# Kernel tuning notes

Measured on AMD Instinct MI355X. Metric: run time of the kernel, lower is better.

## Reference

```python
import jax, jax.numpy as jnp
import numpy as np
import math

T, N, D, H = 1024, 8, 1024, 16
HD = D // H  # head_dim = 64


def setup_inputs() -> dict:
    key = jax.random.key(0)
    k1, k2, k3, k4 = jax.random.split(key, 4)
    scale = 1.0 / math.sqrt(D)  # roughly xavier-scale params
    return {
        "x": jax.random.normal(k1, (T, N, D), dtype=jnp.float32),
        "q_weight": jax.random.normal(k2, (D, H, HD), dtype=jnp.float32) * scale,
        "v_weight": jax.random.normal(k3, (D, H, HD), dtype=jnp.float32) * scale,
        "out_w": jax.random.normal(k4, (D, D), dtype=jnp.float32) * scale,
        "out_b": jnp.zeros((D,), dtype=jnp.float32),
    }


def reference(x, q_weight, v_weight, out_w, out_b):
    inv_sqrt_hd = 1.0 / math.sqrt(HD)
    # q = k : (T, N, H, HD)
    q = jnp.einsum('tbm,mhd->tbhd', x, q_weight)
    q_sq = jnp.einsum('tbhd,tbhd->tbh', q, q)  # squared norms
    # squared L2 distance logits: (T, S, N, H)
    squared_dist = q_sq[:, None] + q_sq[None, :] - 2.0 * jnp.einsum('tbhd,sbhd->tsbh', q, q)
    attn_logits = -squared_dist * inv_sqrt_hd
    attn_weights = jax.nn.softmax(attn_logits, axis=1)  # softmax over source dim S
    # A = W_q W_q^T per head: (H, D, D)
    A = jnp.einsum('mhd,nhd->hmn', q_weight, q_weight) * inv_sqrt_hd
    XA = jnp.einsum('tbm,hmn->tbhn', x, A)           # (T, N, H, D)
    PXA = jnp.einsum('tsbh,sbhm->tbhm', attn_weights, XA)  # (T, N, H, D)
    PXAV = jnp.einsum('tbhm,mhd->tbhd', PXA, v_weight).reshape(T, N, D)
    return PXAV @ out_w.T + out_b
```

## Files before the change

### kernel.cpp

```cpp
#include <hip/hip_runtime.h>
#include <hip/hip_bf16.h>

#define T_ 1024
#define N_ 8
#define D_ 1024
#define H_ 16
#define HD_ 64

typedef __attribute__((ext_vector_type(8))) short bf16x8;
typedef __attribute__((ext_vector_type(2))) float f32x2;
typedef __attribute__((ext_vector_type(4))) float f32x4;
typedef __attribute__((ext_vector_type(16))) float f32x16;
typedef __attribute__((ext_vector_type(4))) int i32x4;
typedef __attribute__((ext_vector_type(2))) int i32x2;
typedef unsigned short u16;
typedef unsigned int u32;

__device__ __forceinline__ float bf2f(u16 u){
  union { float f; unsigned int i; } v; v.i = ((unsigned int)u) << 16; return v.f;
}
__device__ __forceinline__ u16 f2bf(float f){
  union { float f; unsigned int i; } v; v.f = f;
  unsigned int r = v.i + 0x7FFFu + ((v.i >> 16) & 1u);
  return (u16)(r >> 16);
}
__device__ __forceinline__ u16 f2bf_fast(float f){
  __hip_bfloat16 h = __float2bfloat16(f);
  return *reinterpret_cast<u16*>(&h);
}
__device__ __forceinline__ float exp2_raw(float x){
  float r;
  asm("v_exp_f32 %0, %1" : "=v"(r) : "v"(x));
  return r;
}
__device__ __forceinline__ void gl_lds16(const u16* g, u16* l){
  __builtin_amdgcn_global_load_lds(
      (const __attribute__((address_space(1))) unsigned int*)g,
      (__attribute__((address_space(3))) unsigned int*)(unsigned int)(unsigned long long)l,
      16, 0, 0);
}

__global__ __launch_bounds__(256) void k_pre(const float* __restrict__ qw, const float* __restrict__ vw,
                                             float* __restrict__ Bp, const float* __restrict__ Wq,
                                             u16* __restrict__ Wqt){
  __shared__ u16 Qt[64 * 72];
  __shared__ u16 Vt[64 * 72];
  __shared__ float tld[64][65];
  int blk = (int)blockIdx.x;
  int tid = threadIdx.x;
  if (blk < 128){
    int h = blk >> 3, sp = blk & 7;
    int lane = tid & 63, w = tid >> 6;
    int g = lane >> 4, c = lane & 15;
    f32x4 zero = {0.f, 0.f, 0.f, 0.f};
    f32x4 acc[4];
    #pragma unroll
    for (int eb = 0; eb < 4; ++eb) acc[eb] = zero;
    int m = tid >> 2, cg = tid & 3;
    for (int mt = sp * 128; mt < sp * 128 + 128; mt += 64){
      __syncthreads();
      #pragma unroll
      for (int q = 0; q < 4; ++q){
        int e0 = cg * 16 + q * 4;
        f32x4 vq = *(const f32x4*)(qw + (size_t)(mt + m) * D_ + h * 64 + e0);
        f32x4 vv = *(const f32x4*)(vw + (size_t)(mt + m) * D_ + h * 64 + e0);
        #pragma unroll
        for (int j = 0; j < 4; ++j){
          Qt[(e0 + j) * 72 + m] = f2bf_fast(vq[j]);
          Vt[(e0 + j) * 72 + m] = f2bf_fast(vv[j]);
        }
      }
      __syncthreads();
      #pragma unroll
      for (int kk = 0; kk < 2; ++kk){
        bf16x8 av = *(const bf16x8*)&Vt[(w * 16 + c) * 72 + kk * 32 + g * 8];
        #pragma unroll
        for (int eb = 0; eb < 4; ++eb){
          bf16x8 bq = *(const bf16x8*)&Qt[(eb * 16 + c) * 72 + kk * 32 + g * 8];
          acc[eb] = __builtin_amdgcn_mfma_f32_16x16x32_bf16(av, bq, acc[eb], 0, 0, 0);
        }
      }
    }
    #pragma unroll
    for (int eb = 0; eb < 4; ++eb)
      #pragma unroll
      for (int r = 0; r < 4; ++r){
        int d = w * 16 + g * 4 + r, e = eb * 16 + c;
        Bp[(((size_t)sp * 16 + h) * 64 + d) * 64 + e] = acc[eb][r];
      }
  } else {
    int b2 = blk - 128;
    int m0 = (b2 & 15) * 64, n0 = (b2 >> 4) * 64;
    int col = tid & 63, rq = tid >> 6;
    #pragma unroll
    for (int p = 0; p < 16; ++p){
      int row = rq * 16 + p;
      tld[row][col] = Wq[(size_t)(m0 + row) * D_ + n0 + col];
    }
    __syncthreads();
    #pragma unroll
    for (int p = 0; p < 16; ++p){
      int row = rq * 16 + p;
      Wqt[(size_t)(n0 + row) * D_ + m0 + col] = f2bf(tld[col][row]);
    }
  }
}

__global__ __launch_bounds__(256) void k_bred(const float* __restrict__ Bp, u16* __restrict__ Bt){
  int i = blockIdx.x * 256 + threadIdx.x;
  float s = 0.f;
  #pragma unroll
  for (int j = 0; j < 8; ++j) s += Bp[(size_t)j * 65536 + i];
  Bt[i] = f2bf(s * 0.125f);
}

__device__ __forceinline__ int swz(int row, int colbyte){
  return row * 64 + (((colbyte) ^ ((row & 7) << 4)) >> 1);
}

template<int A_F32, int B_F32, int EPI>
__global__ __launch_bounds__(256) void k_gemm(const void* __restrict__ A_, const void* __restrict__ B_,
                                              void* __restrict__ Cv, const float* __restrict__ bias,
                                              int M, int N, int K){
  int nbn = N >> 7;
  int ii = (int)blockIdx.x;
  int sw = (ii & 7) * 64 + (ii >> 3);
  int bm = sw / nbn, bn = sw % nbn;
  int tid = threadIdx.x, lane = tid & 63, wid = tid >> 6;
  int wr = wid >> 1, wc = wid & 1, g = lane >> 4, c = lane & 15;
  __shared__ u16 As[2][128 * 64];
  __shared__ u16 Bs[2][128 * 64];
  int srow[4], scol[4], sdst[4];
  #pragma unroll
  for (int p = 0; p < 4; ++p){
    int slot = (wid * 4 + p) * 64 + lane;
    int row = slot >> 3, c8 = slot & 7;
    srow[p] = row;
    scol[p] = (c8 ^ (row & 7)) * 8;
    sdst[p] = slot * 8;
  }
  int rrow[4], rc8[4];
  #pragma unroll
  for (int p = 0; p < 4; ++p){
    int ci = tid + p * 256;
    rrow[p] = ci >> 3; rc8[p] = ci & 7;
  }
  f32x4 zero = {0.f, 0.f, 0.f, 0.f};
  f32x4 acc[4][4];
  #pragma unroll
  for (int m = 0; m < 4; ++m)
    #pragma unroll
    for (int n = 0; n < 4; ++n) acc[m][n] = zero;
  f32x4 rA[4][2], rB[4][2];
  const u16* Ab = (const u16*)A_;
  const u16* Bb = (const u16*)B_;
  const float* Af = (const float*)A_;
  const float* Bf = (const float*)B_;
  if (!A_F32){
    #pragma unroll
    for (int p = 0; p < 4; ++p)
      gl_lds16(Ab + (size_t)(bm * 128 + srow[p]) * K + scol[p], &As[0][sdst[p]]);
  }
  if (!B_F32){
    #pragma unroll
    for (int p = 0; p < 4; ++p)
      gl_lds16(Bb + (size_t)(bn * 128 + srow[p]) * K + scol[p], &Bs[0][sdst[p]]);
  }
  if (A_F32){
    #pragma unroll
    for (int p = 0; p < 4; ++p){
      const float* src = Af + (size_t)(bm * 128 + rrow[p]) * K + rc8[p] * 8;
      rA[p][0] = *(const f32x4*)src;
      rA[p][1] = *(const f32x4*)(src + 4);
    }
    #pragma unroll
    for (int p = 0; p < 4; ++p){
      union { u16 u[8]; i32x4 v; } pk;
      #pragma unroll
      for (int j = 0; j < 4; ++j){ pk.u[j] = f2bf_fast(rA[p][0][j]); pk.u[4 + j] = f2bf_fast(rA[p][1][j]); }
      *(i32x4*)&As[0][swz(rrow[p], rc8[p] * 16)] = pk.v;
    }
  }
  if (B_F32){
    #pragma unroll
    for (int p = 0; p < 4; ++p){
      const float* src = Bf + (size_t)(bn * 128 + rrow[p]) * K + rc8[p] * 8;
      rB[p][0] = *(const f32x4*)src;
      rB[p][1] = *(const f32x4*)(src + 4);
    }
    #pragma unroll
    for (int p = 0; p < 4; ++p){
      union { u16 u[8]; i32x4 v; } pk;
      #pragma unroll
      for (int j = 0; j < 4; ++j){ pk.u[j] = f2bf_fast(rB[p][0][j]); pk.u[4 + j] = f2bf_fast(rB[p][1][j]); }
      *(i32x4*)&Bs[0][swz(rrow[p], rc8[p] * 16)] = pk.v;
    }
  }
  int NT = K >> 6;
  int cur = 0;
  for (int st = 0; st < NT; ++st){
    __syncthreads();
    int kt1 = (st + 1) * 64;
    int nb = cur ^ 1;
    if (st + 1 < NT){
      if (!A_F32){
        #pragma unroll
        for (int p = 0; p < 4; ++p)
          gl_lds16(Ab + (size_t)(bm * 128 + srow[p]) * K + kt1 + scol[p], &As[nb][sdst[p]]);
      }
      if (!B_F32){
        #pragma unroll
        for (int p = 0; p < 4; ++p)
          gl_lds16(Bb + (size_t)(bn * 128 + srow[p]) * K + kt1 + scol[p], &Bs[nb][sdst[p]]);
      }
      if (A_F32){
        #pragma unroll
        for (int p = 0; p < 4; ++p){
          const float* src = Af + (size_t)(bm * 128 + rrow[p]) * K + kt1 + rc8[p] * 8;
          rA[p][0] = *(const f32x4*)src;
          rA[p][1] = *(const f32x4*)(src + 4);
        }
      }
      if (B_F32){
        #pragma unroll
        for (int p = 0; p < 4; ++p){
          const float* src = Bf + (size_t)(bn * 128 + rrow[p]) * K + kt1 + rc8[p] * 8;
          rB[p][0] = *(const f32x4*)src;
          rB[p][1] = *(const f32x4*)(src + 4);
        }
      }
    }
    #pragma unroll
    for (int kk = 0; kk < 2; ++kk){
      bf16x8 af[4], bfr[4];
      #pragma unroll
      for (int m = 0; m < 4; ++m){
        int row = wr * 64 + m * 16 + c;
        af[m] = *(const bf16x8*)&As[cur][swz(row, kk * 64 + g * 16)];
      }
      #pragma unroll
      for (int n = 0; n < 4; ++n){
        int row = wc * 64 + n * 16 + c;
        bfr[n] = *(const bf16x8*)&Bs[cur][swz(row, kk * 64 + g * 16)];
      }
      #pragma unroll
      for (int m = 0; m < 4; ++m)
        #pragma unroll
        for (int n = 0; n < 4; ++n)
          acc[m][n] = __builtin_amdgcn_mfma_f32_16x16x32_bf16(af[m], bfr[n], acc[m][n], 0, 0, 0);
    }
    if (st + 1 < NT){
      if (A_F32){
        #pragma unroll
        for (int p = 0; p < 4; ++p){
          union { u16 u[8]; i32x4 v; } pk;
          #pragma unroll
          for (int j = 0; j < 4; ++j){ pk.u[j] = f2bf_fast(rA[p][0][j]); pk.u[4 + j] = f2bf_fast(rA[p][1][j]); }
          *(i32x4*)&As[nb][swz(rrow[p], rc8[p] * 16)] = pk.v;
        }
      }
      if (B_F32){
        #pragma unroll
        for (int p = 0; p < 4; ++p){
          union { u16 u[8]; i32x4 v; } pk;
          #pragma unroll
          for (int j = 0; j < 4; ++j){ pk.u[j] = f2bf_fast(rB[p][0][j]); pk.u[4 + j] = f2bf_fast(rB[p][1][j]); }
          *(i32x4*)&Bs[nb][swz(rrow[p], rc8[p] * 16)] = pk.v;
        }
      }
    }
    cur ^= 1;
  }
  #pragma unroll
  for (int m = 0; m < 4; ++m)
    #pragma unroll
    for (int n = 0; n < 4; ++n)
      #pragma unroll
      for (int r = 0; r < 4; ++r){
        int row = bm * 128 + wr * 64 + m * 16 + g * 4 + r;
        int col = bn * 128 + wc * 64 + n * 16 + c;
        float v = acc[m][n][r];
        if (EPI == 0){
          int t = row >> 3, b = row & 7, hh = col >> 6, dd = col & 63;
          ((u16*)Cv)[(((size_t)(b * H_ + hh)) * T_ + t) * HD_ + dd] = f2bf(v);
        } else {
          ((float*)Cv)[(size_t)row * N + col] = v + bias[col];
        }
      }
}

__global__ __launch_bounds__(256) void k_u(const u16* __restrict__ qb, const u16* __restrict__ Bt,
                                           u16* __restrict__ ubt, float* __restrict__ qsq){
  int blk = (int)blockIdx.x;
  int bh = blk >> 2;
  int w = threadIdx.x >> 6;
  int tt = (blk & 3) * 4 + w;
  int h = bh & 15, t0 = tt * 64;
  int lane = threadIdx.x & 63, g = lane >> 4, c = lane & 15;
  const float QS_SCALE = 0.125f * 1.44269504088896340736f;
  bf16x8 af[4][2], bq[4][2];
  #pragma unroll
  for (int mf = 0; mf < 4; ++mf)
    #pragma unroll
    for (int kk = 0; kk < 2; ++kk)
      af[mf][kk] = *(const bf16x8*)(Bt + ((size_t)(h * 64 + mf * 16 + c)) * 64 + kk * 32 + g * 8);
  #pragma unroll
  for (int nf = 0; nf < 4; ++nf)
    #pragma unroll
    for (int kk = 0; kk < 2; ++kk)
      bq[nf][kk] = *(const bf16x8*)(qb + ((size_t)(bh * 1024 + t0 + nf * 16 + c)) * 64 + kk * 32 + g * 8);
  #pragma unroll
  for (int nf = 0; nf < 4; ++nf){
    float ss = 0.f;
    #pragma unroll
    for (int kk = 0; kk < 2; ++kk)
      #pragma unroll
      for (int j = 0; j < 8; ++j){ float f = bf2f((u16)bq[nf][kk][j]); ss = fmaf(f, f, ss); }
    ss += __shfl_xor(ss, 16);
    ss += __shfl_xor(ss, 32);
    if (lane < 16) qsq[(size_t)bh * 1024 + t0 + nf * 16 + lane] = ss * QS_SCALE;
  }
  f32x4 zero = {0.f, 0.f, 0.f, 0.f};
  f32x4 acc[4][4];
  #pragma unroll
  for (int mf = 0; mf < 4; ++mf)
    #pragma unroll
    for (int nf = 0; nf < 4; ++nf) acc[mf][nf] = zero;
  #pragma unroll
  for (int kk = 0; kk < 2; ++kk)
    #pragma unroll
    for (int mf = 0; mf < 4; ++mf)
      #pragma unroll
      for (int nf = 0; nf < 4; ++nf)
        acc[mf][nf] = __builtin_amdgcn_mfma_f32_16x16x32_bf16(af[mf][kk], bq[nf][kk], acc[mf][nf], 0, 0, 0);
  #pragma unroll
  for (int mf = 0; mf < 4; ++mf)
    #pragma unroll
    for (int nf = 0; nf < 4; ++nf)
      #pragma unroll
      for (int r = 0; r < 4; ++r)
        ubt[((size_t)(bh * 64 + mf * 16 + g * 4 + r)) * 1024 + t0 + nf * 16 + c] = f2bf(acc[mf][nf][r]);
}

__global__ __launch_bounds__(512, 2) void k_attn(const u16* __restrict__ qb, const u16* __restrict__ ubt,
                                                 const float* __restrict__ qsq, u16* __restrict__ obm){
  int i = (int)blockIdx.x;
  int bh = ((i & 7) << 4) + (i >> 5);
  int tt = (i >> 3) & 3;
  int b = bh >> 4, h = bh & 15;
  int tid = threadIdx.x, w = tid >> 6, lane = tid & 63;
  int lo = lane & 31, hi = lane >> 5;
  __shared__ u16 Kl[2][64 * 64];
  __shared__ u16 Ul[2][64 * 64];
  __shared__ float Qs[1024];
  const float C1 = 0.25f * 1.44269504088896340736f;
  int t0 = tt * 256 + w * 32;
  const u16* qbh = qb + (size_t)bh * 65536;
  const u16* ubh = ubt + (size_t)bh * 65536;
  const float* qsb = qsq + (size_t)bh * 1024;
  *(f32x2*)&Qs[tid * 2] = *(const f32x2*)(qsb + tid * 2);
  bf16x8 qB[4];
  #pragma unroll
  for (int kd = 0; kd < 4; ++kd)
    qB[kd] = *(const bf16x8*)(qbh + (t0 + lo) * 64 + kd * 16 + hi * 8);
  f32x16 o0 = {0,0,0,0,0,0,0,0,0,0,0,0,0,0,0,0};
  f32x16 o1 = {0,0,0,0,0,0,0,0,0,0,0,0,0,0,0,0};
  const f32x16 zero16 = {0,0,0,0,0,0,0,0,0,0,0,0,0,0,0,0};
  float l_c = 0.f;
  int r0 = tid >> 3, sc0 = ((tid & 7) ^ (r0 & 7)) * 8;
  int d0 = w * 512;
  gl_lds16(qbh + r0 * 64 + sc0, &Kl[0][d0]);
  gl_lds16(ubh + (size_t)r0 * 1024 + sc0, &Ul[0][d0]);
  int cur = 0;
  for (int st = 0; st < 16; ++st){
    int s0 = st * 64;
    __syncthreads();
    if (st < 15){
      int s1 = s0 + 64;
      int nb = cur ^ 1;
      gl_lds16(qbh + (s1 + r0) * 64 + sc0, &Kl[nb][d0]);
      gl_lds16(ubh + (size_t)r0 * 1024 + s1 + sc0, &Ul[nb][d0]);
    }
    const u16* Kc = &Kl[cur][0];
    const u16* Uc = &Ul[cur][0];
    #pragma unroll
    for (int ts = 0; ts < 2; ++ts){
      f32x16 sf = zero16;
      __builtin_amdgcn_s_setprio(1);
      #pragma unroll
      for (int kd = 0; kd < 4; ++kd){
        bf16x8 kA = *(const bf16x8*)&Kc[swz(ts * 32 + lo, kd * 32 + hi * 16)];
        sf = __builtin_amdgcn_mfma_f32_32x32x16_bf16(kA, qB[kd], sf, 0, 0, 0);
      }
      __builtin_amdgcn_s_setprio(0);
      f32x4 qs_[4];
      #pragma unroll
      for (int q = 0; q < 4; ++q)
        qs_[q] = *(const f32x4*)&Qs[s0 + ts * 32 + q * 8 + hi * 4];
      float p[16];
      #pragma unroll
      for (int r = 0; r < 16; ++r)
        p[r] = exp2_raw(fmaf(sf[r], C1, -qs_[r >> 2][r & 3]));
      float sA = ((p[0] + p[1]) + (p[2] + p[3])) + ((p[4] + p[5]) + (p[6] + p[7]));
      float sB = ((p[8] + p[9]) + (p[10] + p[11])) + ((p[12] + p[13]) + (p[14] + p[15]));
      l_c += sA + sB;
      u32 W[8];
      #pragma unroll
      for (int q = 0; q < 8; ++q)
        W[q] = ((u32)f2bf_fast(p[2 * q + 1]) << 16) | (u32)f2bf_fast(p[2 * q]);
      #pragma unroll
      for (int ml = 0; ml < 2; ++ml){
        int m_g = ts * 2 + ml;
        int base = ml * 4;
        i32x2 sw0 = __builtin_amdgcn_permlane32_swap((int)W[base + 0], (int)W[base + 2], false, false);
        i32x2 sw1 = __builtin_amdgcn_permlane32_swap((int)W[base + 1], (int)W[base + 3], false, false);
        union { u32 wd[4]; bf16x8 v; } pa;
        pa.wd[0] = (u32)sw0[0]; pa.wd[1] = (u32)sw1[0]; pa.wd[2] = (u32)sw0[1]; pa.wd[3] = (u32)sw1[1];
        bf16x8 u0 = *(const bf16x8*)&Uc[swz(lo, m_g * 32 + hi * 16)];
        bf16x8 u1 = *(const bf16x8*)&Uc[swz(32 + lo, m_g * 32 + hi * 16)];
        __builtin_amdgcn_s_setprio(1);
        o0 = __builtin_amdgcn_mfma_f32_32x32x16_bf16(pa.v, u0, o0, 0, 0, 0);
        o1 = __builtin_amdgcn_mfma_f32_32x32x16_bf16(pa.v, u1, o1, 0, 0, 0);
        __builtin_amdgcn_s_setprio(0);
      }
    }
    cur ^= 1;
  }
  l_c += __shfl_xor(l_c, 32);
  float inv = 1.0f / l_c;
  #pragma unroll
  for (int r = 0; r < 16; ++r){
    int tr = (r & 3) + 8 * (r >> 2) + 4 * hi;
    float invr = __shfl(inv, tr);
    size_t rowb = ((size_t)((t0 + tr) * 8 + b)) * 1024 + h * 64;
    obm[rowb + lo] = f2bf(o0[r] * invr);
    obm[rowb + 32 + lo] = f2bf(o1[r] * invr);
  }
}

extern "C" void kernel_launch(void* const* d_in, const int* in_sizes, int n_in,
                              void* d_out, int out_size, void* d_ws, size_t ws_size,
                              hipStream_t stream) {
  const float* x   = (const float*)d_in[0];
  const float* qw  = (const float*)d_in[1];
  const float* vw  = (const float*)d_in[2];
  const float* ow  = (const float*)d_in[3];
  const float* ob_bias = (const float*)d_in[4];
  float* out = (float*)d_out;

  float* Bp = (float*)d_out;
  u16* qb  = (u16*)d_out;
  u16* ubt = (u16*)((char*)d_out + (size_t)16 * 1024 * 1024);

  char* ws = (char*)d_ws;
  size_t off = 0;
  auto alloc = [&](size_t bytes) -> void* {
    void* p = ws + off;
    off += (bytes + 255) & ~(size_t)255;
    return p;
  };
  u16*   wqt = (u16*)  alloc((size_t)1024 * 1024 * 2);
  u16*   obm = (u16*)  alloc((size_t)8192 * 1024 * 2);
  float* qsq = (float*)alloc((size_t)128 * 1024 * 4);
  u16*   Bt  = (u16*)  alloc((size_t)16 * 64 * 64 * 2);

  k_pre<<<384, 256, 0, stream>>>(qw, vw, Bp, qw, wqt);
  k_bred<<<256, 256, 0, stream>>>(Bp, Bt);
  k_gemm<1, 0, 0><<<512, 256, 0, stream>>>(x, wqt, qb, nullptr, 8192, 1024, 1024);
  k_u<<<512, 256, 0, stream>>>(qb, Bt, ubt, qsq);
  k_attn<<<512, 512, 0, stream>>>(qb, ubt, qsq, obm);
  k_gemm<0, 1, 1><<<512, 256, 0, stream>>>(obm, ow, out, ob_bias, 8192, 1024, 1024);
}
```

Measured before the change: 121.8 us.

## Fold B reduction into first GEMM launch and double attention staging tile

Removes the separate k_bred launch by giving the first GEMM 16 extra blocks that sum the partial B buffers, with Bp moved to the workspace so it no longer aliases the GEMM output. The attention kernel now loads 128 source rows per double-buffered step instead of 64, which halves the number of barriers and loop iterations. In exchange, LDS use per block roughly doubles, which could limit occupancy, and the reduction blocks add a small tail to the GEMM.

```diff
diff --git a/kernel.cpp b/kernel.cpp
--- a/kernel.cpp
+++ b/kernel.cpp
@@ -106,14 +106,6 @@
   }
 }
 
-__global__ __launch_bounds__(256) void k_bred(const float* __restrict__ Bp, u16* __restrict__ Bt){
-  int i = blockIdx.x * 256 + threadIdx.x;
-  float s = 0.f;
-  #pragma unroll
-  for (int j = 0; j < 8; ++j) s += Bp[(size_t)j * 65536 + i];
-  Bt[i] = f2bf(s * 0.125f);
-}
-
 __device__ __forceinline__ int swz(int row, int colbyte){
   return row * 64 + (((colbyte) ^ ((row & 7) << 4)) >> 1);
 }
@@ -121,9 +113,22 @@
 template<int A_F32, int B_F32, int EPI>
 __global__ __launch_bounds__(256) void k_gemm(const void* __restrict__ A_, const void* __restrict__ B_,
                                               void* __restrict__ Cv, const float* __restrict__ bias,
-                                              int M, int N, int K){
+                                              int M, int N, int K,
+                                              const float* __restrict__ Bp, u16* __restrict__ Bt){
+  int ii = (int)blockIdx.x;
+  if (EPI == 0 && ii >= 512){
+    int base = (ii - 512) * 4096 + threadIdx.x * 16;
+    #pragma unroll 4
+    for (int e = 0; e < 16; ++e){
+      int idx = base + e;
+      float s = 0.f;
+      #pragma unroll
+      for (int j = 0; j < 8; ++j) s += Bp[(size_t)j * 65536 + idx];
+      Bt[idx] = f2bf(s * 0.125f);
+    }
+    return;
+  }
   int nbn = N >> 7;
-  int ii = (int)blockIdx.x;
   int sw = (ii & 7) * 64 + (ii >> 3);
   int bm = sw / nbn, bn = sw % nbn;
   int tid = threadIdx.x, lane = tid & 63, wid = tid >> 6;
@@ -350,8 +355,8 @@
   int b = bh >> 4, h = bh & 15;
   int tid = threadIdx.x, w = tid >> 6, lane = tid & 63;
   int lo = lane & 31, hi = lane >> 5;
-  __shared__ u16 Kl[2][64 * 64];
-  __shared__ u16 Ul[2][64 * 64];
+  __shared__ u16 Kl[2][2][64 * 64];
+  __shared__ u16 Ul[2][2][64 * 64];
   __shared__ float Qs[1024];
   const float C1 = 0.25f * 1.44269504088896340736f;
   int t0 = tt * 256 + w * 32;
@@ -369,59 +374,68 @@
   float l_c = 0.f;
   int r0 = tid >> 3, sc0 = ((tid & 7) ^ (r0 & 7)) * 8;
   int d0 = w * 512;
-  gl_lds16(qbh + r0 * 64 + sc0, &Kl[0][d0]);
-  gl_lds16(ubh + (size_t)r0 * 1024 + sc0, &Ul[0][d0]);
+  #pragma unroll
+  for (int hh = 0; hh < 2; ++hh){
+    gl_lds16(qbh + (hh * 64 + r0) * 64 + sc0, &Kl[0][hh][d0]);
+    gl_lds16(ubh + (size_t)r0 * 1024 + hh * 64 + sc0, &Ul[0][hh][d0]);
+  }
   int cur = 0;
-  for (int st = 0; st < 16; ++st){
-    int s0 = st * 64;
+  for (int st = 0; st < 8; ++st){
     __syncthreads();
-    if (st < 15){
-      int s1 = s0 + 64;
+    if (st < 7){
+      int s1 = (st + 1) * 128;
       int nb = cur ^ 1;
-      gl_lds16(qbh + (s1 + r0) * 64 + sc0, &Kl[nb][d0]);
-      gl_lds16(ubh + (size_t)r0 * 1024 + s1 + sc0, &Ul[nb][d0]);
-    }
-    const u16* Kc = &Kl[cur][0];
-    const u16* Uc = &Ul[cur][0];
-    #pragma unroll
-    for (int ts = 0; ts < 2; ++ts){
-      f32x16 sf = zero16;
-      __builtin_amdgcn_s_setprio(1);
-      #pragma unroll
-      for (int kd = 0; kd < 4; ++kd){
-        bf16x8 kA = *(const bf16x8*)&Kc[swz(ts * 32 + lo, kd * 32 + hi * 16)];
-        sf = __builtin_amdgcn_mfma_f32_32x32x16_bf16(kA, qB[kd], sf, 0, 0, 0);
-      }
-      __builtin_amdgcn_s_setprio(0);
-      f32x4 qs_[4];
-      #pragma unroll
-      for (int q = 0; q < 4; ++q)
-        qs_[q] = *(const f32x4*)&Qs[s0 + ts * 32 + q * 8 + hi * 4];
-      float p[16];
-      #pragma unroll
-      for (int r = 0; r < 16; ++r)
-        p[r] = exp2_raw(fmaf(sf[r], C1, -qs_[r >> 2][r & 3]));
-      float sA = ((p[0] + p[1]) + (p[2] + p[3])) + ((p[4] + p[5]) + (p[6] + p[7]));
-      float sB = ((p[8] + p[9]) + (p[10] + p[11])) + ((p[12] + p[13]) + (p[14] + p[15]));
-      l_c += sA + sB;
-      u32 W[8];
-      #pragma unroll
-      for (int q = 0; q < 8; ++q)
-        W[q] = ((u32)f2bf_fast(p[2 * q + 1]) << 16) | (u32)f2bf_fast(p[2 * q]);
-      #pragma unroll
-      for (int ml = 0; ml < 2; ++ml){
-        int m_g = ts * 2 + ml;
-        int base = ml * 4;
-        i32x2 sw0 = __builtin_amdgcn_permlane32_swap((int)W[base + 0], (int)W[base + 2], false, false);
-        i32x2 sw1 = __builtin_amdgcn_permlane32_swap((int)W[base + 1], (int)W[base + 3], false, false);
-        union { u32 wd[4]; bf16x8 v; } pa;
-        pa.wd[0] = (u32)sw0[0]; pa.wd[1] = (u32)sw1[0]; pa.wd[2] = (u32)sw0[1]; pa.wd[3] = (u32)sw1[1];
-        bf16x8 u0 = *(const bf16x8*)&Uc[swz(lo, m_g * 32 + hi * 16)];
-        bf16x8 u1 = *(const bf16x8*)&Uc[swz(32 + lo, m_g * 32 + hi * 16)];
+      #pragma unroll
+      for (int hh = 0; hh < 2; ++hh){
+        gl_lds16(qbh + (s1 + hh * 64 + r0) * 64 + sc0, &Kl[nb][hh][d0]);
+        gl_lds16(ubh + (size_t)r0 * 1024 + s1 + hh * 64 + sc0, &Ul[nb][hh][d0]);
+      }
+    }
+    #pragma unroll
+    for (int h2 = 0; h2 < 2; ++h2){
+      int s0 = st * 128 + h2 * 64;
+      const u16* Kc = &Kl[cur][h2][0];
+      const u16* Uc = &Ul[cur][h2][0];
+      #pragma unroll
+      for (int ts = 0; ts < 2; ++ts){
+        f32x16 sf = zero16;
         __builtin_amdgcn_s_setprio(1);
-        o0 = __builtin_amdgcn_mfma_f32_32x32x16_bf16(pa.v, u0, o0, 0, 0, 0);
-        o1 = __builtin_amdgcn_mfma_f32_32x32x16_bf16(pa.v, u1, o1, 0, 0, 0);
+        #pragma unroll
+        for (int kd = 0; kd < 4; ++kd){
+          bf16x8 kA = *(const bf16x8*)&Kc[swz(ts * 32 + lo, kd * 32 + hi * 16)];
+          sf = __builtin_amdgcn_mfma_f32_32x32x16_bf16(kA, qB[kd], sf, 0, 0, 0);
+        }
         __builtin_amdgcn_s_setprio(0);
+        f32x4 qs_[4];
+        #pragma unroll
+        for (int q = 0; q < 4; ++q)
+          qs_[q] = *(const f32x4*)&Qs[s0 + ts * 32 + q * 8 + hi * 4];
+        float p[16];
+        #pragma unroll
+        for (int r = 0; r < 16; ++r)
+          p[r] = exp2_raw(fmaf(sf[r], C1, -qs_[r >> 2][r & 3]));
+        float sA = ((p[0] + p[1]) + (p[2] + p[3])) + ((p[4] + p[5]) + (p[6] + p[7]));
+        float sB = ((p[8] + p[9]) + (p[10] + p[11])) + ((p[12] + p[13]) + (p[14] + p[15]));
+        l_c += sA + sB;
+        u32 W[8];
+        #pragma unroll
+        for (int q = 0; q < 8; ++q)
+          W[q] = ((u32)f2bf_fast(p[2 * q + 1]) << 16) | (u32)f2bf_fast(p[2 * q]);
+        #pragma unroll
+        for (int ml = 0; ml < 2; ++ml){
+          int m_g = ts * 2 + ml;
+          int base = ml * 4;
+          i32x2 sw0 = __builtin_amdgcn_permlane32_swap((int)W[base + 0], (int)W[base + 2], false, false);
+          i32x2 sw1 = __builtin_amdgcn_permlane32_swap((int)W[base + 1], (int)W[base + 3], false, false);
+          union { u32 wd[4]; bf16x8 v; } pa;
+          pa.wd[0] = (u32)sw0[0]; pa.wd[1] = (u32)sw1[0]; pa.wd[2] = (u32)sw0[1]; pa.wd[3] = (u32)sw1[1];
+          bf16x8 u0 = *(const bf16x8*)&Uc[swz(lo, m_g * 32 + hi * 16)];
+          bf16x8 u1 = *(const bf16x8*)&Uc[swz(32 + lo, m_g * 32 + hi * 16)];
+          __builtin_amdgcn_s_setprio(1);
+          o0 = __builtin_amdgcn_mfma_f32_32x32x16_bf16(pa.v, u0, o0, 0, 0, 0);
+          o1 = __builtin_amdgcn_mfma_f32_32x32x16_bf16(pa.v, u1, o1, 0, 0, 0);
+          __builtin_amdgcn_s_setprio(0);
+        }
       }
     }
     cur ^= 1;
@@ -448,7 +462,6 @@
   const float* ob_bias = (const float*)d_in[4];
   float* out = (float*)d_out;
 
-  float* Bp = (float*)d_out;
   u16* qb  = (u16*)d_out;
   u16* ubt = (u16*)((char*)d_out + (size_t)16 * 1024 * 1024);
 
@@ -463,11 +476,11 @@
   u16*   obm = (u16*)  alloc((size_t)8192 * 1024 * 2);
   float* qsq = (float*)alloc((size_t)128 * 1024 * 4);
   u16*   Bt  = (u16*)  alloc((size_t)16 * 64 * 64 * 2);
+  float* Bp  = (float*)alloc((size_t)8 * 65536 * 4);
 
   k_pre<<<384, 256, 0, stream>>>(qw, vw, Bp, qw, wqt);
-  k_bred<<<256, 256, 0, stream>>>(Bp, Bt);
-  k_gemm<1, 0, 0><<<512, 256, 0, stream>>>(x, wqt, qb, nullptr, 8192, 1024, 1024);
+  k_gemm<1, 0, 0><<<528, 256, 0, stream>>>(x, wqt, qb, nullptr, 8192, 1024, 1024, Bp, Bt);
   k_u<<<512, 256, 0, stream>>>(qb, Bt, ubt, qsq);
   k_attn<<<512, 512, 0, stream>>>(qb, ubt, qsq, obm);
-  k_gemm<0, 1, 1><<<512, 256, 0, stream>>>(obm, ow, out, ob_bias, 8192, 1024, 1024);
-}
+  k_gemm<0, 1, 1><<<512, 256, 0, stream>>>(obm, ow, out, ob_bias, 8192, 1024, 1024, nullptr, nullptr);
+}
```

Result: slower. 124.5 us (+2.2%).
